# Performance work log

Hardware: AMD Instinct MI355X
Metric: run time of the kernel (lower is better)

Reference implementation:

```python
import jax, jax.numpy as jnp
import numpy as np

W_WIN = 4096   # number of octree windows
K = 32         # patch (window) size
C = 256        # dim
H = 8          # num_heads
D = C // H     # head dim
N = W_WIN * K  # total points
KC = 27        # 3x3x3 octree conv neighborhood
EPS = 1e-5


def layernorm(x, g, b):
    mu = jnp.mean(x, axis=-1, keepdims=True)
    var = jnp.var(x, axis=-1, keepdims=True)
    return (x - mu) * jax.lax.rsqrt(var + EPS) * g + b


def setup_inputs() -> dict:
    key = jax.random.key(0)
    ks = jax.random.split(key, 12)
    s = 0.02
    return {
        'data': jax.random.normal(ks[0], (N, C), jnp.float32),
        'relay_tokens': jax.random.normal(ks[1], (W_WIN, C), jnp.float32),
        'neigh': jax.random.randint(ks[2], (N, KC), 0, N, jnp.int32),
        # CPE: octree depthwise conv (27 taps) + batchnorm (eval, running stats)
        'cpe_w': jax.random.normal(ks[3], (KC, C), jnp.float32) * s,
        'bn_gamma': jnp.ones((C,), jnp.float32),
        'bn_beta': jnp.zeros((C,), jnp.float32),
        'bn_mean': jnp.zeros((C,), jnp.float32),
        'bn_var': jnp.ones((C,), jnp.float32),
        # norm1 / attention
        'norm1_g': jnp.ones((C,), jnp.float32),
        'norm1_b': jnp.zeros((C,), jnp.float32),
        'qkv_w': jax.random.normal(ks[4], (C, 3 * C), jnp.float32) * s,
        'qkv_b': jnp.zeros((3 * C,), jnp.float32),
        'proj_w': jax.random.normal(ks[5], (C, C), jnp.float32) * s,
        'proj_b': jnp.zeros((C,), jnp.float32),
        # norm2 / MLP
        'norm2_g': jnp.ones((C,), jnp.float32),
        'norm2_b': jnp.zeros((C,), jnp.float32),
        'fc1_w': jax.random.normal(ks[6], (C, 4 * C), jnp.float32) * s,
        'fc1_b': jnp.zeros((4 * C,), jnp.float32),
        'fc2_w': jax.random.normal(ks[7], (4 * C, C), jnp.float32) * s,
        'fc2_b': jnp.zeros((C,), jnp.float32),
    }


def _block(data, relay_tokens, neigh, cpe_w, bn_gamma, bn_beta, bn_mean, bn_var,
           norm1_g, norm1_b, qkv_w, qkv_b, proj_w, proj_b,
           norm2_g, norm2_b, fc1_w, fc1_b, fc2_w, fc2_b):
    # ---- CPE: depthwise octree conv + BN, residual ----
    acc = jnp.zeros_like(data)
    for k in range(KC):  # fixed small kernel loop; each gather is [N, C]
        acc = acc + data[neigh[:, k]] * cpe_w[k]
    cpe = (acc - bn_mean) * jax.lax.rsqrt(bn_var + EPS) * bn_gamma + bn_beta
    data = data + cpe

    # ---- data_to_windows + relay-token concat: [W, 1+K, C] ----
    x = data.reshape(W_WIN, K, C)
    x = jnp.concatenate([relay_tokens[:, None, :], x], axis=1)
    S = K + 1

    # ---- windowed MHA over each window (relay token + K points) ----
    h = layernorm(x, norm1_g, norm1_b)
    qkv = (h @ qkv_w + qkv_b).reshape(W_WIN, S, 3, H, D)
    q, kk, v = [jnp.moveaxis(qkv[:, :, i], 2, 1) for i in range(3)]  # [W,H,S,D]
    scale = D ** -0.5
    attn = jax.nn.softmax(jnp.einsum('whsd,whtd->whst', q * scale, kk), axis=-1)
    out = jnp.einsum('whst,whtd->whsd', attn, v)
    out = jnp.moveaxis(out, 1, 2).reshape(W_WIN, S, C)
    x = x + (out @ proj_w + proj_b)  # gamma1 = 1, drop_path = identity

    # ---- MLP residual ----
    h2 = layernorm(x, norm2_g, norm2_b)
    ffn = jax.nn.gelu(h2 @ fc1_w + fc1_b) @ fc2_w + fc2_b
    x = x + ffn  # gamma2 = 1

    # ---- split relay token / windows_to_data ----
    rt = x[:, 0, :]
    data_out = x[:, 1:, :].reshape(N, C)
    return data_out, rt


def reference(data, relay_tokens, neigh, cpe_w, bn_gamma, bn_beta, bn_mean, bn_var,
              norm1_g, norm1_b, qkv_w, qkv_b, proj_w, proj_b,
              norm2_g, norm2_b, fc1_w, fc1_b, fc2_w, fc2_b):
    return _block(data, relay_tokens, neigh, cpe_w, bn_gamma, bn_beta, bn_mean,
                  bn_var, norm1_g, norm1_b, qkv_w, qkv_b, proj_w, proj_b,
                  norm2_g, norm2_b, fc1_w, fc1_b, fc2_w, fc2_b)
```

## Files before the change

### kernel.cpp

```cpp
#include <hip/hip_runtime.h>

#define NW 4096
#define SEQ 33
#define CC 256
#define NTOK 131072
#define NKC 27

typedef unsigned short u16;
typedef __attribute__((ext_vector_type(8))) short s16x8;
typedef __attribute__((ext_vector_type(4))) short s16x4;
typedef __attribute__((ext_vector_type(4))) float f32x4;

#define MFMA16(a,b,c) __builtin_amdgcn_mfma_f32_16x16x32_bf16((a),(b),(c),0,0,0)

__device__ __forceinline__ float bu2f(u16 u){ return __uint_as_float(((unsigned int)u)<<16); }
__device__ __forceinline__ u16 f2bu(float f){
  unsigned int u = __float_as_uint(f);
  return (u16)((u + 0x7FFFu + ((u>>16)&1u)) >> 16);
}

__global__ void k_cvt(const float* __restrict__ in, u16* __restrict__ out, int n4){
  int stride = gridDim.x * blockDim.x;
  for (int i = blockIdx.x*blockDim.x + threadIdx.x; i < n4; i += stride){
    float4 v = ((const float4*)in)[i];
    s16x4 o;
    o[0] = (short)f2bu(v.x); o[1] = (short)f2bu(v.y);
    o[2] = (short)f2bu(v.z); o[3] = (short)f2bu(v.w);
    ((s16x4*)out)[i] = o;
  }
}

__global__ void k_tr(const float* __restrict__ in, u16* __restrict__ out, int R, int C){
  int stride = gridDim.x * blockDim.x;
  int total = R*C;
  for (int i = blockIdx.x*blockDim.x + threadIdx.x; i < total; i += stride){
    int r = i / C, c = i - r*C;
    out[c*R + r] = f2bu(in[i]);
  }
}

__global__ void k_relay(const float* __restrict__ rt, u16* __restrict__ xg){
  int stride = gridDim.x * blockDim.x;
  for (int i = blockIdx.x*blockDim.x + threadIdx.x; i < NW*CC; i += stride){
    int w = i >> 8, c = i & 255;
    xg[(w*SEQ)*CC + c] = f2bu(rt[i]);
  }
}

__global__ void k_cpe(const float* __restrict__ data, const u16* __restrict__ datab,
                      const int* __restrict__ neigh, const float* __restrict__ cpw,
                      const float* __restrict__ bng, const float* __restrict__ bnb,
                      const float* __restrict__ bnm, const float* __restrict__ bnv,
                      u16* __restrict__ xg){
  int n = blockIdx.x*4 + (threadIdx.x >> 6);
  int lane = threadIdx.x & 63;
  int c0 = lane*4;
  float a0=0.f, a1=0.f, a2=0.f, a3=0.f;
  const int* nr = neigh + n*NKC;
  for (int k = 0; k < NKC; ++k){
    int idx = nr[k];
    s16x4 d = *(const s16x4*)(datab + idx*CC + c0);
    float4 wv = *(const float4*)(cpw + k*CC + c0);
    a0 += bu2f((u16)d[0])*wv.x;
    a1 += bu2f((u16)d[1])*wv.y;
    a2 += bu2f((u16)d[2])*wv.z;
    a3 += bu2f((u16)d[3])*wv.w;
  }
  float4 dv = *(const float4*)(data + n*CC + c0);
  float4 g  = *(const float4*)(bng + c0);
  float4 b  = *(const float4*)(bnb + c0);
  float4 m  = *(const float4*)(bnm + c0);
  float4 vv = *(const float4*)(bnv + c0);
  float x0 = dv.x + (a0 - m.x)*rsqrtf(vv.x + 1e-5f)*g.x + b.x;
  float x1 = dv.y + (a1 - m.y)*rsqrtf(vv.y + 1e-5f)*g.y + b.y;
  float x2 = dv.z + (a2 - m.z)*rsqrtf(vv.z + 1e-5f)*g.z + b.z;
  float x3 = dv.w + (a3 - m.w)*rsqrtf(vv.w + 1e-5f)*g.w + b.w;
  int w = n >> 5, s = (n & 31) + 1;
  s16x4 o;
  o[0]=(short)f2bu(x0); o[1]=(short)f2bu(x1); o[2]=(short)f2bu(x2); o[3]=(short)f2bu(x3);
  *(s16x4*)(xg + (w*SEQ + s)*CC + c0) = o;
}

struct SharedT {
  u16 xs[33][264];
  u16 hs[48][264];
  u16 qs[48][40];
  u16 ks[48][40];
  u16 vT[32][72];
  u16 Ps[48][72];
  u16 och[48][40];
  union { float ss[48][52]; u16 mch[48][136]; } u2;
};
static_assert(sizeof(SharedT) <= 80*1024, "LDS budget for 2 blocks/CU");

__global__ __launch_bounds__(256,2) void k_window(
    const u16* __restrict__ xg,
    const u16* __restrict__ qkvT, const u16* __restrict__ projT,
    const u16* __restrict__ fc1T, const u16* __restrict__ fc2T,
    const float* __restrict__ n1g, const float* __restrict__ n1b,
    const float* __restrict__ qkvb, const float* __restrict__ projb,
    const float* __restrict__ n2g, const float* __restrict__ n2b,
    const float* __restrict__ fc1b, const float* __restrict__ fc2b,
    float* __restrict__ out)
{
  __shared__ __align__(16) SharedT L;
  const int tid = threadIdx.x;
  const int lane = tid & 63;
  const int wid = tid >> 6;
  const int l15 = lane & 15;
  const int lg8 = (lane >> 4) * 8;
  const int lg4 = (lane >> 4) * 4;
  const int w = blockIdx.x;
  const f32x4 fzero = {0.f,0.f,0.f,0.f};

  {
    f32x4* p = (f32x4*)&L;
    const int n16 = (int)(sizeof(SharedT)/16);
    for (int i = tid; i < n16; i += 256) p[i] = fzero;
  }
  __syncthreads();

  for (int ci = tid; ci < SEQ*32; ci += 256){
    int r = ci >> 5, cp = (ci & 31) << 3;
    *(s16x8*)&L.xs[r][cp] = *(const s16x8*)(xg + (w*SEQ + r)*CC + cp);
  }
  __syncthreads();

  auto LN = [&](const float* gg, const float* bb){
    for (int r = wid; r < SEQ; r += 4){
      int c0 = lane*4;
      s16x4 xv = *(const s16x4*)&L.xs[r][c0];
      float v0 = bu2f((u16)xv[0]), v1 = bu2f((u16)xv[1]);
      float v2 = bu2f((u16)xv[2]), v3 = bu2f((u16)xv[3]);
      float s  = v0+v1+v2+v3;
      float s2 = v0*v0+v1*v1+v2*v2+v3*v3;
      #pragma unroll
      for (int msk = 1; msk < 64; msk <<= 1){
        s  += __shfl_xor(s, msk);
        s2 += __shfl_xor(s2, msk);
      }
      float mu = s * (1.f/256.f);
      float var = s2 * (1.f/256.f) - mu*mu;
      float rs = rsqrtf(var + 1e-5f);
      float4 gv = *(const float4*)(gg + c0);
      float4 bv = *(const float4*)(bb + c0);
      s16x4 o;
      o[0] = (short)f2bu((v0-mu)*rs*gv.x + bv.x);
      o[1] = (short)f2bu((v1-mu)*rs*gv.y + bv.y);
      o[2] = (short)f2bu((v2-mu)*rs*gv.z + bv.z);
      o[3] = (short)f2bu((v3-mu)*rs*gv.w + bv.w);
      *(s16x4*)&L.hs[r][c0] = o;
    }
  };
  LN(n1g, n1b);
  __syncthreads();

  f32x4 accP[4][3];
  #pragma unroll
  for (int ni = 0; ni < 4; ++ni)
    #pragma unroll
    for (int m = 0; m < 3; ++m) accP[ni][m] = fzero;

  for (int h = 0; h < 8; ++h){
    {
      int nbase = wid + (wid >> 1);
      #pragma unroll
      for (int p = 0; p < 2; ++p){
        int n = nbase + p;
        int m_lo = (p == 0) ? ((wid & 1) ? 2 : 0) : 0;
        int m_hi = (p == 0) ? 2 : ((wid & 1) ? 2 : 1);
        int sel = n >> 1, sub = n & 1;
        int ncol = sel*256 + h*32 + sub*16 + l15;
        const u16* wrow = qkvT + ncol*CC + lg8;
        s16x8 bf[8];
        #pragma unroll
        for (int kk = 0; kk < 8; ++kk) bf[kk] = *(const s16x8*)(wrow + kk*32);
        float bias = qkvb[ncol];
        int colh = sub*16 + l15;
        for (int m = m_lo; m <= m_hi; ++m){
          f32x4 acc = fzero;
          #pragma unroll
          for (int kk = 0; kk < 8; ++kk){
            s16x8 a = *(const s16x8*)&L.hs[m*16 + l15][kk*32 + lg8];
            acc = MFMA16(a, bf[kk], acc);
          }
          int rb = m*16 + lg4;
          #pragma unroll
          for (int jj = 0; jj < 4; ++jj){
            float val = acc[jj] + bias;
            int row = rb + jj;
            if (sel == 0)      L.qs[row][colh] = f2bu(val);
            else if (sel == 1) L.ks[row][colh] = f2bu(val);
            else               L.vT[colh][row] = f2bu(val);
          }
        }
      }
    }
    __syncthreads();
    for (int j = wid; j < 9; j += 4){
      int m = j / 3, n = j - (j/3)*3;
      s16x8 a   = *(const s16x8*)&L.qs[m*16 + l15][lg8];
      s16x8 bfr = *(const s16x8*)&L.ks[n*16 + l15][lg8];
      f32x4 acc = fzero;
      acc = MFMA16(a, bfr, acc);
      int col = n*16 + l15;
      int rb = m*16 + lg4;
      #pragma unroll
      for (int jj = 0; jj < 4; ++jj)
        L.u2.ss[rb + jj][col] = acc[jj] * 0.17677669529663687f;
    }
    __syncthreads();
    for (int r = wid; r < SEQ; r += 4){
      float v = (lane < SEQ) ? L.u2.ss[r][lane] : -1e30f;
      float mx = v;
      #pragma unroll
      for (int msk = 1; msk < 64; msk <<= 1) mx = fmaxf(mx, __shfl_xor(mx, msk));
      float p = (lane < SEQ) ? __expf(v - mx) : 0.f;
      float sm = p;
      #pragma unroll
      for (int msk = 1; msk < 64; msk <<= 1) sm += __shfl_xor(sm, msk);
      L.Ps[r][lane] = f2bu(p / sm);
    }
    __syncthreads();
    for (int j = wid; j < 6; j += 4){
      int m = j >> 1, n = j & 1;
      f32x4 acc = fzero;
      #pragma unroll
      for (int kk = 0; kk < 2; ++kk){
        s16x8 a   = *(const s16x8*)&L.Ps[m*16 + l15][kk*32 + lg8];
        s16x8 bfr = *(const s16x8*)&L.vT[n*16 + l15][kk*32 + lg8];
        acc = MFMA16(a, bfr, acc);
      }
      int col = n*16 + l15;
      int rb = m*16 + lg4;
      #pragma unroll
      for (int jj = 0; jj < 4; ++jj)
        L.och[rb + jj][col] = f2bu(acc[jj]);
    }
    __syncthreads();
    #pragma unroll
    for (int ni = 0; ni < 4; ++ni){
      int n = wid + 4*ni;
      s16x8 bfr = *(const s16x8*)(projT + (n*16 + l15)*CC + h*32 + lg8);
      #pragma unroll
      for (int m = 0; m < 3; ++m){
        s16x8 a = *(const s16x8*)&L.och[m*16 + l15][lg8];
        accP[ni][m] = MFMA16(a, bfr, accP[ni][m]);
      }
    }
  }

  #pragma unroll
  for (int ni = 0; ni < 4; ++ni){
    int col = (wid + 4*ni)*16 + l15;
    float pb = projb[col];
    #pragma unroll
    for (int m = 0; m < 3; ++m){
      #pragma unroll
      for (int jj = 0; jj < 4; ++jj){
        int row = m*16 + lg4 + jj;
        if (row < SEQ){
          float x = bu2f(L.xs[row][col]) + accP[ni][m][jj] + pb;
          L.xs[row][col] = f2bu(x);
        }
      }
    }
  }
  __syncthreads();

  LN(n2g, n2b);
  __syncthreads();

  f32x4 accF[4][3];
  #pragma unroll
  for (int ni = 0; ni < 4; ++ni)
    #pragma unroll
    for (int m = 0; m < 3; ++m) accF[ni][m] = fzero;

  for (int nc = 0; nc < 8; ++nc){
    for (int n = wid; n < 8; n += 4){
      int ncol = nc*128 + n*16 + l15;
      const u16* wrow = fc1T + ncol*CC + lg8;
      s16x8 bf[8];
      #pragma unroll
      for (int kk = 0; kk < 8; ++kk) bf[kk] = *(const s16x8*)(wrow + kk*32);
      float bias = fc1b[ncol];
      int colc = n*16 + l15;
      #pragma unroll
      for (int m = 0; m < 3; ++m){
        f32x4 acc = fzero;
        #pragma unroll
        for (int kk = 0; kk < 8; ++kk){
          s16x8 a = *(const s16x8*)&L.hs[m*16 + l15][kk*32 + lg8];
          acc = MFMA16(a, bf[kk], acc);
        }
        int rb = m*16 + lg4;
        #pragma unroll
        for (int jj = 0; jj < 4; ++jj){
          float xv = acc[jj] + bias;
          float z2 = 1.5957691216057308f*(xv + 0.044715f*xv*xv*xv);
          float gl = xv / (1.f + __expf(-z2));
          L.u2.mch[rb + jj][colc] = f2bu(gl);
        }
      }
    }
    __syncthreads();
    #pragma unroll
    for (int ni = 0; ni < 4; ++ni){
      int n = wid + 4*ni;
      const u16* wrow = fc2T + (n*16 + l15)*1024 + nc*128 + lg8;
      s16x8 bf[4];
      #pragma unroll
      for (int kk = 0; kk < 4; ++kk) bf[kk] = *(const s16x8*)(wrow + kk*32);
      #pragma unroll
      for (int m = 0; m < 3; ++m){
        #pragma unroll
        for (int kk = 0; kk < 4; ++kk){
          s16x8 a = *(const s16x8*)&L.u2.mch[m*16 + l15][kk*32 + lg8];
          accF[ni][m] = MFMA16(a, bf[kk], accF[ni][m]);
        }
      }
    }
    __syncthreads();
  }

  #pragma unroll
  for (int ni = 0; ni < 4; ++ni){
    int col = (wid + 4*ni)*16 + l15;
    float fb = fc2b[col];
    #pragma unroll
    for (int m = 0; m < 3; ++m){
      #pragma unroll
      for (int jj = 0; jj < 4; ++jj){
        int row = m*16 + lg4 + jj;
        if (row < SEQ){
          float x = bu2f(L.xs[row][col]) + accF[ni][m][jj] + fb;
          if (row == 0) out[NTOK*CC + w*CC + col] = x;
          else          out[(w*32 + row - 1)*CC + col] = x;
        }
      }
    }
  }
}

extern "C" void kernel_launch(void* const* d_in, const int* in_sizes, int n_in,
                              void* d_out, int out_size, void* d_ws, size_t ws_size,
                              hipStream_t stream){
  const float* data  = (const float*)d_in[0];
  const float* relay = (const float*)d_in[1];
  const int*   neigh = (const int*)d_in[2];
  const float* cpw   = (const float*)d_in[3];
  const float* bng   = (const float*)d_in[4];
  const float* bnb   = (const float*)d_in[5];
  const float* bnm   = (const float*)d_in[6];
  const float* bnv   = (const float*)d_in[7];
  const float* n1g   = (const float*)d_in[8];
  const float* n1b   = (const float*)d_in[9];
  const float* qkvw  = (const float*)d_in[10];
  const float* qkvb  = (const float*)d_in[11];
  const float* projw = (const float*)d_in[12];
  const float* projb = (const float*)d_in[13];
  const float* n2g   = (const float*)d_in[14];
  const float* n2b   = (const float*)d_in[15];
  const float* fc1w  = (const float*)d_in[16];
  const float* fc1b  = (const float*)d_in[17];
  const float* fc2w  = (const float*)d_in[18];
  const float* fc2b  = (const float*)d_in[19];

  char* ws = (char*)d_ws;
  u16* datab = (u16*)ws;
  u16* xg    = (u16*)(ws + 67108864);
  u16* qkvT  = (u16*)(ws + 136314880);
  u16* projT = (u16*)(ws + 136708096);
  u16* fc1T  = (u16*)(ws + 136839168);
  u16* fc2T  = (u16*)(ws + 137363456);

  k_cvt<<<4096, 256, 0, stream>>>(data, datab, NTOK*CC/4);
  k_tr<<<256, 256, 0, stream>>>(qkvw, qkvT, 256, 768);
  k_tr<<<256, 256, 0, stream>>>(projw, projT, 256, 256);
  k_tr<<<256, 256, 0, stream>>>(fc1w, fc1T, 256, 1024);
  k_tr<<<256, 256, 0, stream>>>(fc2w, fc2T, 1024, 256);
  k_relay<<<1024, 256, 0, stream>>>(relay, xg);
  k_cpe<<<NTOK/4, 256, 0, stream>>>(data, datab, neigh, cpw, bng, bnb, bnm, bnv, xg);
  k_window<<<NW, 256, 0, stream>>>(xg, qkvT, projT, fc1T, fc2T,
                                   n1g, n1b, qkvb, projb, n2g, n2b, fc1b, fc2b,
                                   (float*)d_out);
}
```

Baseline: 1.718 ms.

## Restructure window kernel to 512 threads with all heads processed in parallel

```diff
diff --git a/kernel.cpp b/kernel.cpp
--- a/kernel.cpp
+++ b/kernel.cpp
@@ -81,19 +81,16 @@
   *(s16x4*)(xg + (w*SEQ + s)*CC + c0) = o;
 }
 
-struct SharedT {
+struct SharedW {
   u16 xs[33][264];
-  u16 hs[48][264];
-  u16 qs[48][40];
-  u16 ks[48][40];
-  u16 vT[32][72];
-  u16 Ps[48][72];
-  u16 och[48][40];
-  union { float ss[48][52]; u16 mch[48][136]; } u2;
+  union { u16 hs[48][264]; u16 P[8][33][72]; } A;
+  union { u16 Q[48][264];  u16 och[48][264]; } B;
+  union { u16 K[48][264];  u16 mch[48][264]; } C2;
+  u16 VT[256][72];
 };
-static_assert(sizeof(SharedT) <= 80*1024, "LDS budget for 2 blocks/CU");
-
-__global__ __launch_bounds__(256,2) void k_window(
+static_assert(sizeof(SharedW) <= 160*1024, "LDS budget (1 block/CU)");
+
+__global__ __launch_bounds__(512,2) void k_window(
     const u16* __restrict__ xg,
     const u16* __restrict__ qkvT, const u16* __restrict__ projT,
     const u16* __restrict__ fc1T, const u16* __restrict__ fc2T,
@@ -103,31 +100,29 @@
     const float* __restrict__ fc1b, const float* __restrict__ fc2b,
     float* __restrict__ out)
 {
-  __shared__ __align__(16) SharedT L;
-  const int tid = threadIdx.x;
+  __shared__ __align__(16) SharedW L;
+  const int tid  = threadIdx.x;
   const int lane = tid & 63;
-  const int wid = tid >> 6;
-  const int l15 = lane & 15;
-  const int lg8 = (lane >> 4) * 8;
-  const int lg4 = (lane >> 4) * 4;
-  const int w = blockIdx.x;
+  const int wid  = tid >> 6;
+  const int l15  = lane & 15;
+  const int lg8  = (lane >> 4) * 8;
+  const int lg4  = (lane >> 4) * 4;
+  const int w    = blockIdx.x;
   const f32x4 fzero = {0.f,0.f,0.f,0.f};
 
   {
-    f32x4* p = (f32x4*)&L;
-    const int n16 = (int)(sizeof(SharedT)/16);
-    for (int i = tid; i < n16; i += 256) p[i] = fzero;
-  }
-  __syncthreads();
-
-  for (int ci = tid; ci < SEQ*32; ci += 256){
+    f32x4* p = (f32x4*)((char*)&L + sizeof(L.xs));
+    const int n16 = (int)((sizeof(SharedW) - sizeof(L.xs))/16);
+    for (int i = tid; i < n16; i += 512) p[i] = fzero;
+  }
+  for (int ci = tid; ci < SEQ*32; ci += 512){
     int r = ci >> 5, cp = (ci & 31) << 3;
     *(s16x8*)&L.xs[r][cp] = *(const s16x8*)(xg + (w*SEQ + r)*CC + cp);
   }
   __syncthreads();
 
   auto LN = [&](const float* gg, const float* bb){
-    for (int r = wid; r < SEQ; r += 4){
+    for (int r = wid; r < SEQ; r += 8){
       int c0 = lane*4;
       s16x4 xv = *(const s16x4*)&L.xs[r][c0];
       float v0 = bu2f((u16)xv[0]), v1 = bu2f((u16)xv[1]);
@@ -149,197 +144,239 @@
       o[1] = (short)f2bu((v1-mu)*rs*gv.y + bv.y);
       o[2] = (short)f2bu((v2-mu)*rs*gv.z + bv.z);
       o[3] = (short)f2bu((v3-mu)*rs*gv.w + bv.w);
-      *(s16x4*)&L.hs[r][c0] = o;
+      *(s16x4*)&L.A.hs[r][c0] = o;
     }
   };
   LN(n1g, n1b);
   __syncthreads();
 
-  f32x4 accP[4][3];
+  {
+    s16x8 ahs[3][8];
+    #pragma unroll
+    for (int m = 0; m < 3; ++m)
+      #pragma unroll
+      for (int kk = 0; kk < 8; ++kk)
+        ahs[m][kk] = *(const s16x8*)&L.A.hs[m*16 + l15][kk*32 + lg8];
+    for (int i = 0; i < 6; ++i){
+      int n = wid*6 + i;
+      int sel = n >> 4;
+      int cn  = (n & 15)*16 + l15;
+      int ncol = n*16 + l15;
+      const u16* wrow = qkvT + ncol*CC + lg8;
+      s16x8 bf[8];
+      #pragma unroll
+      for (int kk = 0; kk < 8; ++kk) bf[kk] = *(const s16x8*)(wrow + kk*32);
+      float bias = qkvb[ncol];
+      f32x4 acc[3] = {fzero, fzero, fzero};
+      #pragma unroll
+      for (int kk = 0; kk < 8; ++kk)
+        #pragma unroll
+        for (int m = 0; m < 3; ++m)
+          acc[m] = MFMA16(ahs[m][kk], bf[kk], acc[m]);
+      #pragma unroll
+      for (int m = 0; m < 3; ++m)
+        #pragma unroll
+        for (int jj = 0; jj < 4; ++jj){
+          int row = m*16 + lg4 + jj;
+          float val = acc[m][jj] + bias;
+          if (sel == 0)      L.B.Q[row][cn]  = f2bu(val*0.17677669529663687f);
+          else if (sel == 1) L.C2.K[row][cn] = f2bu(val);
+          else               L.VT[cn][row]   = f2bu(val);
+        }
+    }
+  }
+  __syncthreads();
+
+  {
+    const int h = wid;
+    {
+      s16x8 z = {0,0,0,0,0,0,0,0};
+      for (int i = lane; i < 66; i += 64){
+        int r = i >> 1, c = 48 + (i & 1)*8;
+        *(s16x8*)&L.A.P[h][r][c] = z;
+      }
+    }
+    s16x8 aq[3], bk[3];
+    #pragma unroll
+    for (int m = 0; m < 3; ++m) aq[m] = *(const s16x8*)&L.B.Q[m*16 + l15][h*32 + lg8];
+    #pragma unroll
+    for (int n = 0; n < 3; ++n) bk[n] = *(const s16x8*)&L.C2.K[n*16 + l15][h*32 + lg8];
+    f32x4 sc[3][3];
+    #pragma unroll
+    for (int m = 0; m < 3; ++m)
+      #pragma unroll
+      for (int n = 0; n < 3; ++n)
+        sc[m][n] = MFMA16(aq[m], bk[n], fzero);
+    #pragma unroll
+    for (int m = 0; m < 3; ++m)
+      #pragma unroll
+      for (int jj = 0; jj < 4; ++jj){
+        float a0 = sc[m][0][jj];
+        float a1 = sc[m][1][jj];
+        float a2 = (l15 == 0) ? sc[m][2][jj] : -1e30f;
+        float mx = fmaxf(fmaxf(a0, a1), a2);
+        #pragma unroll
+        for (int msk = 1; msk < 16; msk <<= 1) mx = fmaxf(mx, __shfl_xor(mx, msk));
+        float e0 = __expf(a0 - mx), e1 = __expf(a1 - mx), e2 = __expf(a2 - mx);
+        float sm = e0 + e1 + e2;
+        #pragma unroll
+        for (int msk = 1; msk < 16; msk <<= 1) sm += __shfl_xor(sm, msk);
+        float inv = 1.f / sm;
+        int row = m*16 + lg4 + jj;
+        if (row < SEQ){
+          L.A.P[h][row][l15]      = f2bu(e0*inv);
+          L.A.P[h][row][16 + l15] = f2bu(e1*inv);
+          L.A.P[h][row][32 + l15] = f2bu(e2*inv);
+        }
+      }
+  }
+  __syncthreads();
+
+  {
+    const int h = wid;
+    s16x8 pa[3][2];
+    #pragma unroll
+    for (int m = 0; m < 3; ++m){
+      int row = m*16 + l15; if (row > 32) row = 32;
+      pa[m][0] = *(const s16x8*)&L.A.P[h][row][lg8];
+      pa[m][1] = *(const s16x8*)&L.A.P[h][row][32 + lg8];
+    }
+    f32x4 acc[2][3];
+    #pragma unroll
+    for (int n = 0; n < 2; ++n){
+      s16x8 bv0 = *(const s16x8*)&L.VT[h*32 + n*16 + l15][lg8];
+      s16x8 bv1 = *(const s16x8*)&L.VT[h*32 + n*16 + l15][32 + lg8];
+      #pragma unroll
+      for (int m = 0; m < 3; ++m){
+        f32x4 a = MFMA16(pa[m][0], bv0, fzero);
+        acc[n][m] = MFMA16(pa[m][1], bv1, a);
+      }
+    }
+    #pragma unroll
+    for (int n = 0; n < 2; ++n)
+      #pragma unroll
+      for (int m = 0; m < 3; ++m)
+        #pragma unroll
+        for (int jj = 0; jj < 4; ++jj)
+          L.B.och[m*16 + lg4 + jj][h*32 + n*16 + l15] = f2bu(acc[n][m][jj]);
+  }
+  __syncthreads();
+
+  {
+    s16x8 ao[3][8];
+    #pragma unroll
+    for (int m = 0; m < 3; ++m)
+      #pragma unroll
+      for (int kk = 0; kk < 8; ++kk)
+        ao[m][kk] = *(const s16x8*)&L.B.och[m*16 + l15][kk*32 + lg8];
+    #pragma unroll
+    for (int i = 0; i < 2; ++i){
+      int ncol = (wid*2 + i)*16 + l15;
+      const u16* wrow = projT + ncol*CC + lg8;
+      s16x8 bf[8];
+      #pragma unroll
+      for (int kk = 0; kk < 8; ++kk) bf[kk] = *(const s16x8*)(wrow + kk*32);
+      f32x4 acc[3] = {fzero, fzero, fzero};
+      #pragma unroll
+      for (int kk = 0; kk < 8; ++kk)
+        #pragma unroll
+        for (int m = 0; m < 3; ++m)
+          acc[m] = MFMA16(ao[m][kk], bf[kk], acc[m]);
+      float pb = projb[ncol];
+      #pragma unroll
+      for (int m = 0; m < 3; ++m)
+        #pragma unroll
+        for (int jj = 0; jj < 4; ++jj){
+          int row = m*16 + lg4 + jj;
+          if (row < SEQ){
+            float x = bu2f(L.xs[row][ncol]) + acc[m][jj] + pb;
+            L.xs[row][ncol] = f2bu(x);
+          }
+        }
+    }
+  }
+  __syncthreads();
+
+  LN(n2g, n2b);
+  __syncthreads();
+
+  f32x4 accF[2][3];
   #pragma unroll
-  for (int ni = 0; ni < 4; ++ni)
-    #pragma unroll
-    for (int m = 0; m < 3; ++m) accP[ni][m] = fzero;
-
-  for (int h = 0; h < 8; ++h){
-    {
-      int nbase = wid + (wid >> 1);
-      #pragma unroll
-      for (int p = 0; p < 2; ++p){
-        int n = nbase + p;
-        int m_lo = (p == 0) ? ((wid & 1) ? 2 : 0) : 0;
-        int m_hi = (p == 0) ? 2 : ((wid & 1) ? 2 : 1);
-        int sel = n >> 1, sub = n & 1;
-        int ncol = sel*256 + h*32 + sub*16 + l15;
-        const u16* wrow = qkvT + ncol*CC + lg8;
+  for (int i = 0; i < 2; ++i)
+    #pragma unroll
+    for (int m = 0; m < 3; ++m) accF[i][m] = fzero;
+
+  {
+    s16x8 ah2[3][8];
+    #pragma unroll
+    for (int m = 0; m < 3; ++m)
+      #pragma unroll
+      for (int kk = 0; kk < 8; ++kk)
+        ah2[m][kk] = *(const s16x8*)&L.A.hs[m*16 + l15][kk*32 + lg8];
+
+    for (int nc = 0; nc < 4; ++nc){
+      #pragma unroll
+      for (int i = 0; i < 2; ++i){
+        int nl = (wid*2 + i)*16 + l15;
+        int ncol = nc*256 + nl;
+        const u16* wrow = fc1T + ncol*CC + lg8;
         s16x8 bf[8];
         #pragma unroll
         for (int kk = 0; kk < 8; ++kk) bf[kk] = *(const s16x8*)(wrow + kk*32);
-        float bias = qkvb[ncol];
-        int colh = sub*16 + l15;
-        for (int m = m_lo; m <= m_hi; ++m){
-          f32x4 acc = fzero;
+        float bias = fc1b[ncol];
+        f32x4 acc[3] = {fzero, fzero, fzero};
+        #pragma unroll
+        for (int kk = 0; kk < 8; ++kk)
           #pragma unroll
-          for (int kk = 0; kk < 8; ++kk){
-            s16x8 a = *(const s16x8*)&L.hs[m*16 + l15][kk*32 + lg8];
-            acc = MFMA16(a, bf[kk], acc);
-          }
-          int rb = m*16 + lg4;
+          for (int m = 0; m < 3; ++m)
+            acc[m] = MFMA16(ah2[m][kk], bf[kk], acc[m]);
+        #pragma unroll
+        for (int m = 0; m < 3; ++m)
           #pragma unroll
           for (int jj = 0; jj < 4; ++jj){
-            float val = acc[jj] + bias;
-            int row = rb + jj;
-            if (sel == 0)      L.qs[row][colh] = f2bu(val);
-            else if (sel == 1) L.ks[row][colh] = f2bu(val);
-            else               L.vT[colh][row] = f2bu(val);
+            int row = m*16 + lg4 + jj;
+            float xv = acc[m][jj] + bias;
+            float z2 = 1.5957691216057308f*(xv + 0.044715f*xv*xv*xv);
+            float gl = xv / (1.f + __expf(-z2));
+            L.C2.mch[row][nl] = f2bu(gl);
           }
-        }
-      }
-    }
-    __syncthreads();
-    for (int j = wid; j < 9; j += 4){
-      int m = j / 3, n = j - (j/3)*3;
-      s16x8 a   = *(const s16x8*)&L.qs[m*16 + l15][lg8];
-      s16x8 bfr = *(const s16x8*)&L.ks[n*16 + l15][lg8];
-      f32x4 acc = fzero;
-      acc = MFMA16(a, bfr, acc);
-      int col = n*16 + l15;
-      int rb = m*16 + lg4;
-      #pragma unroll
-      for (int jj = 0; jj < 4; ++jj)
-        L.u2.ss[rb + jj][col] = acc[jj] * 0.17677669529663687f;
-    }
-    __syncthreads();
-    for (int r = wid; r < SEQ; r += 4){
-      float v = (lane < SEQ) ? L.u2.ss[r][lane] : -1e30f;
-      float mx = v;
-      #pragma unroll
-      for (int msk = 1; msk < 64; msk <<= 1) mx = fmaxf(mx, __shfl_xor(mx, msk));
-      float p = (lane < SEQ) ? __expf(v - mx) : 0.f;
-      float sm = p;
-      #pragma unroll
-      for (int msk = 1; msk < 64; msk <<= 1) sm += __shfl_xor(sm, msk);
-      L.Ps[r][lane] = f2bu(p / sm);
-    }
-    __syncthreads();
-    for (int j = wid; j < 6; j += 4){
-      int m = j >> 1, n = j & 1;
-      f32x4 acc = fzero;
-      #pragma unroll
-      for (int kk = 0; kk < 2; ++kk){
-        s16x8 a   = *(const s16x8*)&L.Ps[m*16 + l15][kk*32 + lg8];
-        s16x8 bfr = *(const s16x8*)&L.vT[n*16 + l15][kk*32 + lg8];
-        acc = MFMA16(a, bfr, acc);
-      }
-      int col = n*16 + l15;
-      int rb = m*16 + lg4;
-      #pragma unroll
-      for (int jj = 0; jj < 4; ++jj)
-        L.och[rb + jj][col] = f2bu(acc[jj]);
-    }
-    __syncthreads();
-    #pragma unroll
-    for (int ni = 0; ni < 4; ++ni){
-      int n = wid + 4*ni;
-      s16x8 bfr = *(const s16x8*)(projT + (n*16 + l15)*CC + h*32 + lg8);
-      #pragma unroll
-      for (int m = 0; m < 3; ++m){
-        s16x8 a = *(const s16x8*)&L.och[m*16 + l15][lg8];
-        accP[ni][m] = MFMA16(a, bfr, accP[ni][m]);
-      }
+      }
+      __syncthreads();
+      {
+        const u16* wr0 = fc2T + ((wid*2 + 0)*16 + l15)*1024 + nc*256 + lg8;
+        const u16* wr1 = fc2T + ((wid*2 + 1)*16 + l15)*1024 + nc*256 + lg8;
+        s16x8 b0[8], b1[8];
+        #pragma unroll
+        for (int kk = 0; kk < 8; ++kk){ b0[kk] = *(const s16x8*)(wr0 + kk*32);
+                                        b1[kk] = *(const s16x8*)(wr1 + kk*32); }
+        #pragma unroll
+        for (int kk = 0; kk < 8; ++kk)
+          #pragma unroll
+          for (int m = 0; m < 3; ++m){
+            s16x8 a = *(const s16x8*)&L.C2.mch[m*16 + l15][kk*32 + lg8];
+            accF[0][m] = MFMA16(a, b0[kk], accF[0][m]);
+            accF[1][m] = MFMA16(a, b1[kk], accF[1][m]);
+          }
+      }
+      __syncthreads();
     }
   }
 
   #pragma unroll
-  for (int ni = 0; ni < 4; ++ni){
-    int col = (wid + 4*ni)*16 + l15;
-    float pb = projb[col];
-    #pragma unroll
-    for (int m = 0; m < 3; ++m){
+  for (int i = 0; i < 2; ++i){
+    int col = (wid*2 + i)*16 + l15;
+    float fb = fc2b[col];
+    #pragma unroll
+    for (int m = 0; m < 3; ++m)
       #pragma unroll
       for (int jj = 0; jj < 4; ++jj){
         int row = m*16 + lg4 + jj;
         if (row < SEQ){
-          float x = bu2f(L.xs[row][col]) + accP[ni][m][jj] + pb;
-          L.xs[row][col] = f2bu(x);
-        }
-      }
-    }
-  }
-  __syncthreads();
-
-  LN(n2g, n2b);
-  __syncthreads();
-
-  f32x4 accF[4][3];
-  #pragma unroll
-  for (int ni = 0; ni < 4; ++ni)
-    #pragma unroll
-    for (int m = 0; m < 3; ++m) accF[ni][m] = fzero;
-
-  for (int nc = 0; nc < 8; ++nc){
-    for (int n = wid; n < 8; n += 4){
-      int ncol = nc*128 + n*16 + l15;
-      const u16* wrow = fc1T + ncol*CC + lg8;
-      s16x8 bf[8];
-      #pragma unroll
-      for (int kk = 0; kk < 8; ++kk) bf[kk] = *(const s16x8*)(wrow + kk*32);
-      float bias = fc1b[ncol];
-      int colc = n*16 + l15;
-      #pragma unroll
-      for (int m = 0; m < 3; ++m){
-        f32x4 acc = fzero;
-        #pragma unroll
-        for (int kk = 0; kk < 8; ++kk){
-          s16x8 a = *(const s16x8*)&L.hs[m*16 + l15][kk*32 + lg8];
-          acc = MFMA16(a, bf[kk], acc);
-        }
-        int rb = m*16 + lg4;
-        #pragma unroll
-        for (int jj = 0; jj < 4; ++jj){
-          float xv = acc[jj] + bias;
-          float z2 = 1.5957691216057308f*(xv + 0.044715f*xv*xv*xv);
-          float gl = xv / (1.f + __expf(-z2));
-          L.u2.mch[rb + jj][colc] = f2bu(gl);
-        }
-      }
-    }
-    __syncthreads();
-    #pragma unroll
-    for (int ni = 0; ni < 4; ++ni){
-      int n = wid + 4*ni;
-      const u16* wrow = fc2T + (n*16 + l15)*1024 + nc*128 + lg8;
-      s16x8 bf[4];
-      #pragma unroll
-      for (int kk = 0; kk < 4; ++kk) bf[kk] = *(const s16x8*)(wrow + kk*32);
-      #pragma unroll
-      for (int m = 0; m < 3; ++m){
-        #pragma unroll
-        for (int kk = 0; kk < 4; ++kk){
-          s16x8 a = *(const s16x8*)&L.u2.mch[m*16 + l15][kk*32 + lg8];
-          accF[ni][m] = MFMA16(a, bf[kk], accF[ni][m]);
-        }
-      }
-    }
-    __syncthreads();
-  }
-
-  #pragma unroll
-  for (int ni = 0; ni < 4; ++ni){
-    int col = (wid + 4*ni)*16 + l15;
-    float fb = fc2b[col];
-    #pragma unroll
-    for (int m = 0; m < 3; ++m){
-      #pragma unroll
-      for (int jj = 0; jj < 4; ++jj){
-        int row = m*16 + lg4 + jj;
-        if (row < SEQ){
-          float x = bu2f(L.xs[row][col]) + accF[ni][m][jj] + fb;
+          float x = bu2f(L.xs[row][col]) + accF[i][m][jj] + fb;
           if (row == 0) out[NTOK*CC + w*CC + col] = x;
           else          out[(w*32 + row - 1)*CC + col] = x;
         }
       }
-    }
   }
 }
 
@@ -382,7 +419,7 @@
   k_tr<<<256, 256, 0, stream>>>(fc2w, fc2T, 1024, 256);
   k_relay<<<1024, 256, 0, stream>>>(relay, xg);
   k_cpe<<<NTOK/4, 256, 0, stream>>>(data, datab, neigh, cpw, bng, bnb, bnm, bnv, xg);
-  k_window<<<NW, 256, 0, stream>>>(xg, qkvT, projT, fc1T, fc2T,
+  k_window<<<NW, 512, 0, stream>>>(xg, qkvT, projT, fc1T, fc2T,
                                    n1g, n1b, qkvb, projb, n2g, n2b, fc1b, fc2b,
                                    (float*)d_out);
 }
```

Measured after the change: 1.541 ms. 1.11x faster.
